# Performance work log

Hardware: AMD Instinct MI355X
Metric: run time of the kernel (lower is better)

Reference implementation:

```python
import jax, jax.numpy as jnp
import numpy as np

N_NODES = 32768
N_EDGES = 524288
IN_CH = 128
OUT_CH = 128
EDGE_CH = 64
HIDDEN = 128


def setup_inputs() -> dict:
    key = jax.random.key(0)
    ks = jax.random.split(key, 8)
    x = jax.random.normal(ks[0], (N_NODES, IN_CH), dtype=jnp.float32)
    edge_index = jax.random.randint(ks[1], (2, N_EDGES), 0, N_NODES, dtype=jnp.int64)
    edge_attr = jax.random.uniform(ks[2], (N_EDGES, EDGE_CH), dtype=jnp.float32)
    # filter_network: Linear(edge_ch, hidden) -> tanh -> Linear(hidden, out)
    s1 = 1.0 / np.sqrt(EDGE_CH)
    s2 = 1.0 / np.sqrt(HIDDEN)
    W1 = jax.random.uniform(ks[3], (EDGE_CH, HIDDEN), jnp.float32, -s1, s1)
    b1 = jax.random.uniform(ks[4], (HIDDEN,), jnp.float32, -s1, s1)
    W2 = jax.random.uniform(ks[5], (HIDDEN, OUT_CH), jnp.float32, -s2, s2)
    b2 = jax.random.uniform(ks[6], (OUT_CH,), jnp.float32, -s2, s2)
    # attention_vector [out, 1], xavier_uniform with gain 1.414
    lim = 1.414 * np.sqrt(6.0 / (OUT_CH + 1))
    attn = jax.random.uniform(ks[7], (OUT_CH,), jnp.float32, -lim, lim)
    return {"x": x, "edge_index": edge_index, "edge_attr": edge_attr,
            "W1": W1, "b1": b1, "W2": W2, "b2": b2, "attn": attn}


def _segment_softmax(scores, segment_ids, num_segments):
    # PyG-style numerically stable softmax over segments
    seg_max = jax.ops.segment_max(scores, segment_ids, num_segments=num_segments)
    seg_max = jnp.where(jnp.isfinite(seg_max), seg_max, 0.0)
    e = jnp.exp(scores - seg_max[segment_ids])
    denom = jax.ops.segment_sum(e, segment_ids, num_segments=num_segments)
    return e / (denom[segment_ids] + 1e-16)


def reference(x, edge_index, edge_attr, W1, b1, W2, b2, attn):
    source, target = edge_index[0], edge_index[1]
    n_nodes = x.shape[0]
    source_features = x[source]                                  # [E, in]
    edge_attr_norm = edge_attr / (jnp.linalg.norm(edge_attr, axis=-1, keepdims=True) + 1e-8)
    h = jnp.tanh(edge_attr_norm @ W1 + b1)                       # [E, hidden]
    edge_filters = h @ W2 + b2                                   # [E, out]
    messages = source_features * edge_filters                    # [E, out]
    attention_scores = messages @ attn                           # [E]
    attention_weights = _segment_softmax(attention_scores, target, n_nodes)
    messages = messages * attention_weights[:, None]
    output = jax.ops.segment_sum(messages, target, num_segments=n_nodes)  # [N, out]
    return output, attention_weights
```

## Files before the change

### kernel.cpp

```cpp
#include <hip/hip_runtime.h>
#include <stdint.h>

typedef short short8 __attribute__((ext_vector_type(8)));
typedef float f32x16 __attribute__((ext_vector_type(16)));

__device__ __forceinline__ unsigned cvtpk(float lo, float hi){
  unsigned r;
  asm("v_cvt_pk_bf16_f32 %0, %1, %2" : "=v"(r) : "v"(lo), "v"(hi));
  return r;
}

__device__ __forceinline__ short8 frag_from(unsigned a, unsigned b, unsigned c, unsigned d){
  union { unsigned u[4]; short8 s; } t;
  t.u[0] = a; t.u[1] = b; t.u[2] = c; t.u[3] = d;
  return t.s;
}

__global__ void k_prep(const float* __restrict__ W1, const float* __restrict__ W2,
                       uint4* __restrict__ Wf)
{
  const int t = blockIdx.x * 256 + threadIdx.x;
  if (t >= 48 * 64) return;
  const int f = t >> 6, l = t & 63;
  const int r = l & 31, hh = l >> 5;
  float v[8];
  if (f < 16) {
    const int mf = f >> 2, ks = f & 3;
    const int c = 32 * mf + r, kb = ks * 16 + hh * 8;
#pragma unroll
    for (int j = 0; j < 8; ++j) v[j] = W1[(kb + j) * 128 + c];
  } else {
    const int f2 = f - 16, mf2 = f2 >> 3, ks = f2 & 7;
    const int o = 32 * mf2 + r, cb = ks * 16 + hh * 8;
#pragma unroll
    for (int j = 0; j < 8; ++j) v[j] = W2[(cb + j) * 128 + o];
  }
  uint4 d;
  d.x = cvtpk(v[0], v[1]); d.y = cvtpk(v[2], v[3]);
  d.z = cvtpk(v[4], v[5]); d.w = cvtpk(v[6], v[7]);
  Wf[(long long)f * 64 + l] = d;
}

__global__ void k_hist(const int* __restrict__ ei, int* __restrict__ rowptr, int E){
  for (long long i = (long long)blockIdx.x * 256 + threadIdx.x; i < E;
       i += (long long)gridDim.x * 256)
    atomicAdd(&rowptr[ei[E + i]], 1);
}

__global__ __launch_bounds__(1024)
void k_scan(int* __restrict__ p, int N){
  __shared__ int ls[1024];
  const int t = threadIdx.x;
  const int chunk = (N + 1023) >> 10;
  const int c0 = t * chunk, c1 = min(N, c0 + chunk);
  int s = 0;
  for (int i = c0; i < c1; ++i) s += p[i];
  ls[t] = s;
  __syncthreads();
  for (int off = 1; off < 1024; off <<= 1) {
    int add = (t >= off) ? ls[t - off] : 0;
    __syncthreads();
    ls[t] += add;
    __syncthreads();
  }
  int run = (t == 0) ? 0 : ls[t - 1];
  for (int i = c0; i < c1; ++i) { int v = p[i]; p[i] = run; run += v; }
}

__global__ void k_fill(const int* __restrict__ ei, int* __restrict__ rowptr,
                       int* __restrict__ pose, int E){
  for (long long i = (long long)blockIdx.x * 256 + threadIdx.x; i < E;
       i += (long long)gridDim.x * 256) {
    int tg = ei[E + i];
    pose[i] = atomicAdd(&rowptr[tg], 1);
  }
}

__global__ __launch_bounds__(256)
void k1_fused(const float* __restrict__ x, const int* __restrict__ ei,
              const float* __restrict__ ea, const uint4* __restrict__ Wf,
              const float* __restrict__ b1, const float* __restrict__ b2,
              const float* __restrict__ attn, const int* __restrict__ pose,
              unsigned* __restrict__ msgp, float* __restrict__ scoreS,
              float* __restrict__ scorig, int E)
{
  const int lane = threadIdx.x & 63;
  const int wv   = threadIdx.x >> 6;
  const int h    = lane >> 5;
  const int r31  = lane & 31;
  const long long e   = (long long)blockIdx.x * 128 + wv * 32 + r31;
  const long long eld = (e < E) ? e : (long long)(E - 1);

  const int pos = pose[eld];
  const int src = ei[eld];

  float av[32];
  const float* earow = ea + eld * 64 + h * 8;
#pragma unroll
  for (int ks = 0; ks < 4; ++ks) {
    float4 p0 = *(const float4*)(earow + ks * 16);
    float4 p1 = *(const float4*)(earow + ks * 16 + 4);
    av[ks*8+0] = p0.x; av[ks*8+1] = p0.y; av[ks*8+2] = p0.z; av[ks*8+3] = p0.w;
    av[ks*8+4] = p1.x; av[ks*8+5] = p1.y; av[ks*8+6] = p1.z; av[ks*8+7] = p1.w;
  }
  float ss = 0.f;
#pragma unroll
  for (int i = 0; i < 32; ++i) ss = fmaf(av[i], av[i], ss);
  ss += __shfl_xor(ss, 32);
  const float rin = 1.0f / (sqrtf(ss) + 1e-8f);

  unsigned eb[4][4];
#pragma unroll
  for (int ks = 0; ks < 4; ++ks)
#pragma unroll
    for (int d = 0; d < 4; ++d)
      eb[ks][d] = cvtpk(av[ks*8+2*d] * rin, av[ks*8+2*d+1] * rin);

  const float* xrow = x + (long long)src * 128;
  float4 xA[8];
#pragma unroll
  for (int i = 0; i < 8; ++i) {
    const int mf2 = i >> 2, rq = i & 3;
    xA[i] = *(const float4*)(xrow + 32*mf2 + 8*rq + 4*h);
  }
  asm volatile("" ::: "memory");

  unsigned hb[8][4];
#pragma unroll
  for (int mf = 0; mf < 4; ++mf) {
    f32x16 a1;
#pragma unroll
    for (int i = 0; i < 16; ++i) a1[i] = 0.f;
#pragma unroll
    for (int ks = 0; ks < 4; ++ks) {
      uint4 w = Wf[(mf * 4 + ks) * 64 + lane];
      a1 = __builtin_amdgcn_mfma_f32_32x32x16_bf16(
          frag_from(w.x, w.y, w.z, w.w),
          frag_from(eb[ks][0], eb[ks][1], eb[ks][2], eb[ks][3]), a1, 0, 0, 0);
    }
    float hv[16];
#pragma unroll
    for (int rq = 0; rq < 4; ++rq) {
      float4 bc = *(const float4*)(b1 + 32*mf + 8*rq + 4*h);
#pragma unroll
      for (int i = 0; i < 4; ++i) {
        float pre = a1[rq*4+i] + ((const float*)&bc)[i];
        float e2  = __expf(2.0f * pre);
        hv[rq*4+i] = 1.0f - 2.0f / (e2 + 1.0f);
      }
    }
#pragma unroll
    for (int q = 0; q < 2; ++q) {
      unsigned A = cvtpk(hv[q*8+0], hv[q*8+1]);
      unsigned B = cvtpk(hv[q*8+2], hv[q*8+3]);
      unsigned C = cvtpk(hv[q*8+4], hv[q*8+5]);
      unsigned D = cvtpk(hv[q*8+6], hv[q*8+7]);
      unsigned Axr = (unsigned)__shfl_xor((int)A, 32);
      unsigned Bxr = (unsigned)__shfl_xor((int)B, 32);
      unsigned Cxr = (unsigned)__shfl_xor((int)C, 32);
      unsigned Dxr = (unsigned)__shfl_xor((int)D, 32);
      hb[2*mf+q][0] = h ? Cxr : A;
      hb[2*mf+q][1] = h ? Dxr : B;
      hb[2*mf+q][2] = h ? C   : Axr;
      hb[2*mf+q][3] = h ? D   : Bxr;
    }
  }

  float4 xB[8];
#pragma unroll
  for (int i = 0; i < 8; ++i) {
    const int mf2 = 2 + (i >> 2), rq = i & 3;
    xB[i] = *(const float4*)(xrow + 32*mf2 + 8*rq + 4*h);
  }
  asm volatile("" ::: "memory");

  float score = 0.f;
#pragma unroll
  for (int mf2 = 0; mf2 < 4; ++mf2) {
    f32x16 a2;
#pragma unroll
    for (int i = 0; i < 16; ++i) a2[i] = 0.f;
#pragma unroll
    for (int ks = 0; ks < 8; ++ks) {
      uint4 w = Wf[(16 + mf2 * 8 + ks) * 64 + lane];
      a2 = __builtin_amdgcn_mfma_f32_32x32x16_bf16(
          frag_from(w.x, w.y, w.z, w.w),
          frag_from(hb[ks][0], hb[ks][1], hb[ks][2], hb[ks][3]), a2, 0, 0, 0);
    }
    unsigned pk[8];
#pragma unroll
    for (int rq = 0; rq < 4; ++rq) {
      const int o0 = 32*mf2 + 8*rq + 4*h;
      float4 b2c = *(const float4*)(b2 + o0);
      float4 atc = *(const float4*)(attn + o0);
      float4 xc  = (mf2 < 2) ? xA[mf2*4+rq] : xB[(mf2-2)*4+rq];
      float m0 = (a2[rq*4+0] + b2c.x) * xc.x;
      float m1 = (a2[rq*4+1] + b2c.y) * xc.y;
      float m2 = (a2[rq*4+2] + b2c.z) * xc.z;
      float m3 = (a2[rq*4+3] + b2c.w) * xc.w;
      score = fmaf(m0, atc.x, score);
      score = fmaf(m1, atc.y, score);
      score = fmaf(m2, atc.z, score);
      score = fmaf(m3, atc.w, score);
      pk[2*rq]   = cvtpk(m0, m1);
      pk[2*rq+1] = cvtpk(m2, m3);
    }
    if (e < E) {
      uint4* dst = (uint4*)(msgp + (long long)pos * 64 + 16*mf2 + 8*h);
      uint4 s0, s1;
      s0.x = pk[0]; s0.y = pk[1]; s0.z = pk[2]; s0.w = pk[3];
      s1.x = pk[4]; s1.y = pk[5]; s1.z = pk[6]; s1.w = pk[7];
      dst[0] = s0; dst[1] = s1;
    }
  }
  score += __shfl_xor(score, 32);
  if (h == 0 && e < E) {
    scoreS[pos] = score;
    scorig[e]   = score;
  }
}

__global__ __launch_bounds__(256)
void k_gather(const unsigned* __restrict__ msgp, const float* __restrict__ scoreS,
              const int* __restrict__ rowptr, float* __restrict__ lse,
              float* __restrict__ out, int N)
{
  const int lane = threadIdx.x & 63;
  const int node = blockIdx.x * 4 + (threadIdx.x >> 6);
  if (node >= N) return;
  const int end   = rowptr[node];
  const int start = node ? rowptr[node - 1] : 0;
  const int L     = end - start;

  float m = -3.4e38f, s = 0.f;
  for (int c0 = 0; c0 < L; c0 += 64) {
    const int j = c0 + lane;
    float sc = (j < L) ? scoreS[start + j] : -3.4e38f;
    float cm = sc;
#pragma unroll
    for (int off = 32; off; off >>= 1) cm = fmaxf(cm, __shfl_xor(cm, off));
    const float mn = fmaxf(m, cm);
    float ex = (j < L) ? __expf(sc - mn) : 0.f;
#pragma unroll
    for (int off = 32; off; off >>= 1) ex += __shfl_xor(ex, off);
    s = s * __expf(m - mn) + ex;
    m = mn;
  }
  const float lsev = m + logf(s + 1e-16f);
  if (lane == 0) lse[node] = lsev;

  float2 acc; acc.x = 0.f; acc.y = 0.f;
  for (int c0 = 0; c0 < L; c0 += 64) {
    const int j = c0 + lane;
    float w = (j < L) ? __expf(scoreS[start + j] - lsev) : 0.f;
    const int jn = min(64, L - c0);
#pragma unroll 4
    for (int j2 = 0; j2 < jn; ++j2) {
      float wj = __shfl(w, j2);
      unsigned md = msgp[(long long)(start + c0 + j2) * 64 + lane];
      acc.x = fmaf(wj, __uint_as_float(md << 16),          acc.x);
      acc.y = fmaf(wj, __uint_as_float(md & 0xffff0000u), acc.y);
    }
  }
  const int mf2 = lane >> 4, hh = (lane >> 3) & 1, rq = (lane >> 1) & 3, half = lane & 1;
  const int ch0 = 32*mf2 + 8*rq + 4*hh + 2*half;
  *(float2*)(out + (long long)node * 128 + ch0) = acc;
}

__global__ void k_wfin(float* __restrict__ wbuf, const int* __restrict__ ei,
                       const float* __restrict__ lse, int E){
  for (long long i = (long long)blockIdx.x * 256 + threadIdx.x; i < E;
       i += (long long)gridDim.x * 256) {
    float scv = wbuf[i];
    int tg = ei[E + i];
    wbuf[i] = __expf(scv - lse[tg]);
  }
}

extern "C" void kernel_launch(void* const* d_in, const int* in_sizes, int n_in,
                              void* d_out, int out_size, void* d_ws, size_t ws_size,
                              hipStream_t stream)
{
  const float* x    = (const float*)d_in[0];
  const int*   ei   = (const int*)d_in[1];
  const float* ea   = (const float*)d_in[2];
  const float* W1   = (const float*)d_in[3];
  const float* b1   = (const float*)d_in[4];
  const float* W2   = (const float*)d_in[5];
  const float* b2   = (const float*)d_in[6];
  const float* attn = (const float*)d_in[7];
  const int N = in_sizes[0] / 128;
  const int E = in_sizes[2] / 64;
  if (E <= 0 || N <= 0) return;

  float* out   = (float*)d_out;
  float* wregN = out + (long long)N * 128;
  uint4* Wf    = (uint4*)d_out;

  char* wsb = (char*)d_ws;
  unsigned* msgp   = (unsigned*)wsb;
  float*    scoreS = (float*)(wsb + (size_t)E * 256);
  int*      rowptr = (int*)(wsb + (size_t)E * 256 + (size_t)E * 4);
  float*    lse    = (float*)(wsb + (size_t)E * 260 + (size_t)N * 4);
  const size_t need = (size_t)E * 260 + (size_t)N * 8;
  if (ws_size < need) return;

  hipMemsetAsync(rowptr, 0, (size_t)N * 4, stream);
  k_prep<<<12, 256, 0, stream>>>(W1, W2, Wf);
  k_hist<<<1024, 256, 0, stream>>>(ei, rowptr, E);
  k_scan<<<1, 1024, 0, stream>>>(rowptr, N);
  k_fill<<<1024, 256, 0, stream>>>(ei, rowptr, (int*)wregN, E);
  k1_fused<<<(E + 127) / 128, 256, 0, stream>>>(x, ei, ea, Wf, b1, b2, attn,
                                                (const int*)wregN, msgp, scoreS,
                                                wregN, E);
  k_gather<<<(N + 3) / 4, 256, 0, stream>>>(msgp, scoreS, rowptr, lse, out, N);
  k_wfin<<<1024, 256, 0, stream>>>(wregN, ei, lse, E);
}
```

Before: 281.7 us.

## Iterate fused edge kernel in target-sorted order via inverse permutation

k_fill now also writes an inverse permutation (sorted position to original edge id) into the output buffer. The fused MFMA kernel iterates over sorted positions and gathers edge_attr and source index through it, so message and score stores become contiguous instead of scattered. The original-order score copy is dropped, and k_wfin now reads the sorted score through the stored position. In exchange, edge_attr reads (256 B per edge) become random gathers, and the output region is reused as scratch for the permutation.

New measurement: 295.2 us. 1.05x slower.

```diff
diff --git a/kernel.cpp b/kernel.cpp
--- a/kernel.cpp
+++ b/kernel.cpp
@@ -3,6 +3,7 @@
 
 typedef short short8 __attribute__((ext_vector_type(8)));
 typedef float f32x16 __attribute__((ext_vector_type(16)));
+typedef unsigned ux4 __attribute__((ext_vector_type(4)));
 
 __device__ __forceinline__ unsigned cvtpk(float lo, float hi){
   unsigned r;
@@ -17,7 +18,7 @@
 }
 
 __global__ void k_prep(const float* __restrict__ W1, const float* __restrict__ W2,
-                       uint4* __restrict__ Wf)
+                       ux4* __restrict__ Wf)
 {
   const int t = blockIdx.x * 256 + threadIdx.x;
   if (t >= 48 * 64) return;
@@ -35,7 +36,7 @@
 #pragma unroll
     for (int j = 0; j < 8; ++j) v[j] = W2[(cb + j) * 128 + o];
   }
-  uint4 d;
+  ux4 d;
   d.x = cvtpk(v[0], v[1]); d.y = cvtpk(v[2], v[3]);
   d.z = cvtpk(v[4], v[5]); d.w = cvtpk(v[6], v[7]);
   Wf[(long long)f * 64 + l] = d;
@@ -68,34 +69,36 @@
 }
 
 __global__ void k_fill(const int* __restrict__ ei, int* __restrict__ rowptr,
-                       int* __restrict__ pose, int E){
+                       int* __restrict__ pose, int* __restrict__ eidx, int E){
   for (long long i = (long long)blockIdx.x * 256 + threadIdx.x; i < E;
        i += (long long)gridDim.x * 256) {
     int tg = ei[E + i];
-    pose[i] = atomicAdd(&rowptr[tg], 1);
+    int pos = atomicAdd(&rowptr[tg], 1);
+    pose[i] = pos;
+    eidx[pos] = (int)i;
   }
 }
 
 __global__ __launch_bounds__(256)
 void k1_fused(const float* __restrict__ x, const int* __restrict__ ei,
-              const float* __restrict__ ea, const uint4* __restrict__ Wf,
+              const float* __restrict__ ea, const ux4* __restrict__ Wf,
               const float* __restrict__ b1, const float* __restrict__ b2,
-              const float* __restrict__ attn, const int* __restrict__ pose,
-              unsigned* __restrict__ msgp, float* __restrict__ scoreS,
-              float* __restrict__ scorig, int E)
+              const float* __restrict__ attn, const int* __restrict__ eidx,
+              unsigned* __restrict__ msgp, float* __restrict__ scoreS, int E)
 {
   const int lane = threadIdx.x & 63;
   const int wv   = threadIdx.x >> 6;
   const int h    = lane >> 5;
   const int r31  = lane & 31;
-  const long long e   = (long long)blockIdx.x * 128 + wv * 32 + r31;
-  const long long eld = (e < E) ? e : (long long)(E - 1);
-
-  const int pos = pose[eld];
-  const int src = ei[eld];
+  const long long p   = (long long)blockIdx.x * 128 + wv * 32 + r31;
+  const long long pld = (p < E) ? p : (long long)(E - 1);
+
+  const int e   = eidx[pld];
+  const int src = ei[e];
+  const float* xrow = x + (long long)src * 128;
 
   float av[32];
-  const float* earow = ea + eld * 64 + h * 8;
+  const float* earow = ea + (long long)e * 64 + h * 8;
 #pragma unroll
   for (int ks = 0; ks < 4; ++ks) {
     float4 p0 = *(const float4*)(earow + ks * 16);
@@ -116,7 +119,6 @@
     for (int d = 0; d < 4; ++d)
       eb[ks][d] = cvtpk(av[ks*8+2*d] * rin, av[ks*8+2*d+1] * rin);
 
-  const float* xrow = x + (long long)src * 128;
   float4 xA[8];
 #pragma unroll
   for (int i = 0; i < 8; ++i) {
@@ -133,7 +135,7 @@
     for (int i = 0; i < 16; ++i) a1[i] = 0.f;
 #pragma unroll
     for (int ks = 0; ks < 4; ++ks) {
-      uint4 w = Wf[(mf * 4 + ks) * 64 + lane];
+      ux4 w = Wf[(mf * 4 + ks) * 64 + lane];
       a1 = __builtin_amdgcn_mfma_f32_32x32x16_bf16(
           frag_from(w.x, w.y, w.z, w.w),
           frag_from(eb[ks][0], eb[ks][1], eb[ks][2], eb[ks][3]), a1, 0, 0, 0);
@@ -182,7 +184,7 @@
     for (int i = 0; i < 16; ++i) a2[i] = 0.f;
 #pragma unroll
     for (int ks = 0; ks < 8; ++ks) {
-      uint4 w = Wf[(16 + mf2 * 8 + ks) * 64 + lane];
+      ux4 w = Wf[(16 + mf2 * 8 + ks) * 64 + lane];
       a2 = __builtin_amdgcn_mfma_f32_32x32x16_bf16(
           frag_from(w.x, w.y, w.z, w.w),
           frag_from(hb[ks][0], hb[ks][1], hb[ks][2], hb[ks][3]), a2, 0, 0, 0);
@@ -205,19 +207,16 @@
       pk[2*rq]   = cvtpk(m0, m1);
       pk[2*rq+1] = cvtpk(m2, m3);
     }
-    if (e < E) {
-      uint4* dst = (uint4*)(msgp + (long long)pos * 64 + 16*mf2 + 8*h);
-      uint4 s0, s1;
+    if (p < E) {
+      ux4* dst = (ux4*)(msgp + p * 64 + 16*mf2 + 8*h);
+      ux4 s0, s1;
       s0.x = pk[0]; s0.y = pk[1]; s0.z = pk[2]; s0.w = pk[3];
       s1.x = pk[4]; s1.y = pk[5]; s1.z = pk[6]; s1.w = pk[7];
       dst[0] = s0; dst[1] = s1;
     }
   }
   score += __shfl_xor(score, 32);
-  if (h == 0 && e < E) {
-    scoreS[pos] = score;
-    scorig[e]   = score;
-  }
+  if (h == 0 && p < E) scoreS[p] = score;
 }
 
 __global__ __launch_bounds__(256)
@@ -267,13 +266,14 @@
   *(float2*)(out + (long long)node * 128 + ch0) = acc;
 }
 
-__global__ void k_wfin(float* __restrict__ wbuf, const int* __restrict__ ei,
-                       const float* __restrict__ lse, int E){
+__global__ void k_wfin(int* __restrict__ pw, const int* __restrict__ ei,
+                       const float* __restrict__ scoreS, const float* __restrict__ lse,
+                       int E){
   for (long long i = (long long)blockIdx.x * 256 + threadIdx.x; i < E;
        i += (long long)gridDim.x * 256) {
-    float scv = wbuf[i];
-    int tg = ei[E + i];
-    wbuf[i] = __expf(scv - lse[tg]);
+    int pos = pw[i];
+    float w = __expf(scoreS[pos] - lse[ei[E + i]]);
+    pw[i] = __float_as_int(w);
   }
 }
 
@@ -295,7 +295,8 @@
 
   float* out   = (float*)d_out;
   float* wregN = out + (long long)N * 128;
-  uint4* Wf    = (uint4*)d_out;
+  ux4*   Wf    = (ux4*)d_out;
+  int*   eidx  = (int*)((char*)d_out + 65536);
 
   char* wsb = (char*)d_ws;
   unsigned* msgp   = (unsigned*)wsb;
@@ -304,15 +305,16 @@
   float*    lse    = (float*)(wsb + (size_t)E * 260 + (size_t)N * 4);
   const size_t need = (size_t)E * 260 + (size_t)N * 8;
   if (ws_size < need) return;
-
-  hipMemsetAsync(rowptr, 0, (size_t)N * 4, stream);
+  if ((size_t)out_size < (size_t)N * 128 + (size_t)E) return;
+  if ((size_t)N * 128 * 4 < 65536 + (size_t)E * 4) return;
+
+  (void)hipMemsetAsync(rowptr, 0, (size_t)N * 4, stream);
   k_prep<<<12, 256, 0, stream>>>(W1, W2, Wf);
   k_hist<<<1024, 256, 0, stream>>>(ei, rowptr, E);
   k_scan<<<1, 1024, 0, stream>>>(rowptr, N);
-  k_fill<<<1024, 256, 0, stream>>>(ei, rowptr, (int*)wregN, E);
+  k_fill<<<1024, 256, 0, stream>>>(ei, rowptr, (int*)wregN, eidx, E);
   k1_fused<<<(E + 127) / 128, 256, 0, stream>>>(x, ei, ea, Wf, b1, b2, attn,
-                                                (const int*)wregN, msgp, scoreS,
-                                                wregN, E);
+                                                eidx, msgp, scoreS, E);
   k_gather<<<(N + 3) / 4, 256, 0, stream>>>(msgp, scoreS, rowptr, lse, out, N);
-  k_wfin<<<1024, 256, 0, stream>>>(wregN, ei, lse, E);
-}
+  k_wfin<<<1024, 256, 0, stream>>>((int*)wregN, ei, scoreS, lse, E);
+}
```
